# Kernel tuning notes

Hardware: AMD Instinct MI355X
Metric: run time of the kernel (lower is better)

Reference implementation:

```python
import jax, jax.numpy as jnp
import numpy as np

DIM = 768
NUM_HEADS = 12
HEAD_DIM = DIM // NUM_HEADS
SCALE = HEAD_DIM ** -0.5
B, N = 4, 2048


def setup_inputs() -> dict:
    key = jax.random.key(0)
    k1, k2, k3 = jax.random.split(key, 3)
    x = jax.random.normal(k1, (B, N, DIM), dtype=jnp.float32)
    W_qk = jax.random.normal(k2, (2 * DIM, DIM), dtype=jnp.float32) * (DIM ** -0.5)
    b_qk = jax.random.normal(k3, (2 * DIM,), dtype=jnp.float32) * 0.02
    return {"x": x, "W_qk": W_qk, "b_qk": b_qk}


def reference(x, W_qk, b_qk):
    Bb, Nn, C = x.shape
    # qk projection: [B,N,2C] -> [B,N,2,H,D] -> q,k each [B,H,N,D]
    qk = x @ W_qk.T + b_qk
    qk = qk.reshape(Bb, Nn, 2, NUM_HEADS, HEAD_DIM).transpose(2, 0, 3, 1, 4)
    q, k = qk[0], qk[1]
    # attention scores [B,H,N,N]
    attn = jnp.einsum("bhnd,bhmd->bhnm", q, k) * SCALE
    attn = jax.nn.softmax(attn, axis=-1)
    # mean over heads, then per-query diagonal -> [B,N]
    attn_weights = jnp.diagonal(attn.mean(axis=1), axis1=-2, axis2=-1)
    return attn_weights
```

## Files before the change

kernel.cpp:

```cpp
#include <hip/hip_runtime.h>
#include <math.h>


#define B_ 4
#define N_ 2048
#define H_ 12
#define D_ 64
#define C_ 768
#define TWO_C 1536
#define QSCALE 0.18033688011112043f

typedef _Float16 half8 __attribute__((ext_vector_type(8)));
typedef _Float16 half4 __attribute__((ext_vector_type(4)));
typedef float floatx4 __attribute__((ext_vector_type(4)));

#if __has_builtin(__builtin_amdgcn_exp2f)
#define EXP2(x) __builtin_amdgcn_exp2f(x)
#else
#define EXP2(x) exp2f(x)
#endif

__device__ __forceinline__ void gload_lds16(const _Float16* g, _Float16* l) {
  __builtin_amdgcn_global_load_lds(
      (const __attribute__((address_space(1))) void*)g,
      (__attribute__((address_space(3))) void*)l, 16, 0, 0);
}

#define NX4 1572864
#define NW4 294912
__global__ __launch_bounds__(256) void conv_kernel(const float* __restrict__ x,
                                                   const float* __restrict__ W,
                                                   _Float16* __restrict__ xh,
                                                   _Float16* __restrict__ wh) {
  int i = blockIdx.x * 256 + threadIdx.x;
  const float* in;
  _Float16* out;
  int idx;
  if (i < NX4) {
    in = x; out = xh; idx = i;
  } else if (i < NX4 + NW4) {
    in = W; out = wh; idx = i - NX4;
  } else {
    return;
  }
  float4 v = ((const float4*)in)[idx];
  half4 o;
  o[0] = (_Float16)v.x; o[1] = (_Float16)v.y;
  o[2] = (_Float16)v.z; o[3] = (_Float16)v.w;
  ((half4*)out)[idx] = o;
}

__global__ __launch_bounds__(256) void proj_kernel(
    const _Float16* __restrict__ xh, const _Float16* __restrict__ wh,
    const float* __restrict__ bias, _Float16* __restrict__ qh,
    _Float16* __restrict__ kh) {
  __shared__ _Float16 As[128 * 32];
  __shared__ _Float16 Bs[128 * 32];
  const int t = threadIdx.x;
  const int l = t & 63;
  const int w = t >> 6;
  const int wr = w >> 1, wc = w & 1;

  int lin = blockIdx.y * 12 + blockIdx.x;
  int swz = (lin & 7) * 96 + (lin >> 3);
  const int bm = (swz / 12) * 128;
  const int bc = (swz % 12) * 128;

  const int srow = l >> 2;
  const int schunk = (l & 3) ^ ((l >> 3) & 3);

  floatx4 acc[4][4] = {};

  for (int k0 = 0; k0 < C_; k0 += 32) {
    __syncthreads();
#pragma unroll
    for (int i = 0; i < 2; ++i) {
      int rbase = w * 32 + i * 16;
      const _Float16* ga =
          xh + (size_t)(bm + rbase + srow) * C_ + k0 + schunk * 8;
      gload_lds16(ga, As + rbase * 32);
      const _Float16* gb =
          wh + (size_t)(bc + rbase + srow) * C_ + k0 + schunk * 8;
      gload_lds16(gb, Bs + rbase * 32);
    }
    __syncthreads();

    half8 af[4], bf[4];
#pragma unroll
    for (int fr = 0; fr < 4; ++fr) {
      int row = wr * 64 + fr * 16 + (l & 15);
      int ch = (l >> 4) ^ ((row >> 1) & 3);
      af[fr] = *(const half8*)(As + row * 32 + ch * 8);
    }
#pragma unroll
    for (int fc = 0; fc < 4; ++fc) {
      int row = wc * 64 + fc * 16 + (l & 15);
      int ch = (l >> 4) ^ ((row >> 1) & 3);
      bf[fc] = *(const half8*)(Bs + row * 32 + ch * 8);
    }
#pragma unroll
    for (int fr = 0; fr < 4; ++fr)
#pragma unroll
      for (int fc = 0; fc < 4; ++fc)
        acc[fr][fc] = __builtin_amdgcn_mfma_f32_16x16x32_f16(
            af[fr], bf[fc], acc[fr][fc], 0, 0, 0);
  }

#pragma unroll
  for (int fr = 0; fr < 4; ++fr) {
#pragma unroll
    for (int fc = 0; fc < 4; ++fc) {
#pragma unroll
      for (int j = 0; j < 4; ++j) {
        int m = bm + wr * 64 + fr * 16 + ((l >> 4) << 2) + j;
        int c = bc + wc * 64 + fc * 16 + (l & 15);
        float v = acc[fr][fc][j] + bias[c];
        int b = m >> 11, n = m & (N_ - 1);
        int cc = (c < C_) ? c : c - C_;
        if (c < C_) v *= QSCALE;
        int hh = cc >> 6, d = cc & 63;
        _Float16* dst = (c < C_) ? qh : kh;
        dst[((((size_t)b * H_ + hh) * N_ + n) << 6) + d] = (_Float16)v;
      }
    }
  }
}

__global__ __launch_bounds__(256) void attn_kernel(
    const _Float16* __restrict__ qh, const _Float16* __restrict__ kh,
    float* __restrict__ part) {
  __shared__ _Float16 ks[4][64 * 64];
  const int t = threadIdx.x;
  const int l = t & 63;
  const int w = t >> 6;

  int lin = blockIdx.x;
  int swz = (lin & 7) * 192 + (lin >> 3);
  const int qt = swz & 31;
  const int h = (swz >> 5) % 12;
  const int b = swz / 384;

  const _Float16* qb = qh + (((size_t)(b * H_ + h) * N_ + qt * 64) << 6);
  const _Float16* kb = kh + (((size_t)(b * H_ + h) * N_) << 6);

  half8 qf[4][2];
#pragma unroll
  for (int fr = 0; fr < 4; ++fr)
#pragma unroll
    for (int kd = 0; kd < 2; ++kd)
      qf[fr][kd] = *(const half8*)(qb + (size_t)(fr * 16 + (l & 15)) * 64 +
                                   kd * 32 + (l >> 4) * 8);

  const int lin0 = w * 64 + l;
  const int row0 = lin0 >> 3, slot0 = lin0 & 7;
  const int soff0 = row0 * 64 + (slot0 ^ (row0 & 7)) * 8;
  const int lin1 = lin0 + 256;
  const int row1 = lin1 >> 3, slot1 = lin1 & 7;
  const int soff1 = row1 * 64 + (slot1 ^ (row1 & 7)) * 8;

#define STAGE(KT)                                                   \
  {                                                                 \
    const _Float16* kp_ = kb + (size_t)(KT) * 4096;                 \
    _Float16* ld_ = ks[(KT) & 3];                                   \
    gload_lds16(kp_ + soff0, ld_ + w * 512);                        \
    gload_lds16(kp_ + soff1, ld_ + w * 512 + 2048);                 \
  }

  const int frow = w * 16 + (l & 15);
  const int koff0 = frow * 64 + (((l >> 4) + 0) ^ (l & 7)) * 8;
  const int koff1 = frow * 64 + (((l >> 4) + 4) ^ (l & 7)) * 8;

  float lsum[4][4] = {};
  float ed[4] = {0.f, 0.f, 0.f, 0.f};

  STAGE(0);
  STAGE(1);
  STAGE(2);

#define ITER(KT, VMASM, DO_STAGE)                                             \
  {                                                                           \
    asm volatile(VMASM ::: "memory");                                         \
    __builtin_amdgcn_s_barrier();                                             \
    asm volatile("" ::: "memory");                                            \
    const _Float16* bufp = ks[(KT) & 3];                                      \
    half8 kf0 = *(const half8*)(bufp + koff0);                                \
    half8 kf1 = *(const half8*)(bufp + koff1);                                \
    if (DO_STAGE) STAGE((KT) + 3);                                            \
    floatx4 acc[4] = {};                                                      \
    _Pragma("unroll") for (int fr = 0; fr < 4; ++fr) {                        \
      acc[fr] = __builtin_amdgcn_mfma_f32_16x16x32_f16(qf[fr][0], kf0,        \
                                                       acc[fr], 0, 0, 0);     \
      acc[fr] = __builtin_amdgcn_mfma_f32_16x16x32_f16(qf[fr][1], kf1,        \
                                                       acc[fr], 0, 0, 0);     \
    }                                                                         \
    _Pragma("unroll") for (int fr = 0; fr < 4; ++fr)                          \
        _Pragma("unroll") for (int j = 0; j < 4; ++j) {                       \
      float e = EXP2(acc[fr][j]);                                             \
      lsum[fr][j] += e;                                                       \
    }                                                                         \
    if ((KT) == qt) {                                                         \
      _Pragma("unroll") for (int fr = 0; fr < 4; ++fr)                        \
          _Pragma("unroll") for (int j = 0; j < 4; ++j) {                     \
        if (fr == w && (l & 15) == (((l >> 4) << 2) + j))                     \
          ed[j] = EXP2(acc[fr][j]);                                           \
      }                                                                       \
    }                                                                         \
  }

  for (int kt = 0; kt < 29; ++kt) ITER(kt, "s_waitcnt vmcnt(4)", true);
  ITER(29, "s_waitcnt vmcnt(4)", false);
  ITER(30, "s_waitcnt vmcnt(2)", false);
  ITER(31, "s_waitcnt vmcnt(0)", false);
#undef ITER
#undef STAGE

#pragma unroll
  for (int fr = 0; fr < 4; ++fr)
#pragma unroll
    for (int j = 0; j < 4; ++j)
#pragma unroll
      for (int m = 1; m < 16; m <<= 1)
        lsum[fr][j] += __shfl_xor(lsum[fr][j], m, 16);
#pragma unroll
  for (int j = 0; j < 4; ++j)
#pragma unroll
    for (int m = 1; m < 16; m <<= 1) ed[j] += __shfl_xor(ed[j], m, 16);

  __builtin_amdgcn_s_barrier();
  float* red = (float*)ks[0];
  float* edl = red + 256;
  if ((l & 15) == 0) {
#pragma unroll
    for (int fr = 0; fr < 4; ++fr)
#pragma unroll
      for (int j = 0; j < 4; ++j)
        red[w * 64 + fr * 16 + ((l >> 4) << 2) + j] = lsum[fr][j];
#pragma unroll
    for (int j = 0; j < 4; ++j) edl[w * 16 + ((l >> 4) << 2) + j] = ed[j];
  }
  __syncthreads();

  if (t < 64) {
    float ls = red[t] + red[64 + t] + red[128 + t] + red[192 + t];
    part[(size_t)(b * H_ + h) * N_ + qt * 64 + t] = edl[t] / ls;
  }
}

__global__ __launch_bounds__(256) void reduce_kernel(
    const float* __restrict__ part, float* __restrict__ out) {
  int g = blockIdx.x * 256 + threadIdx.x;
  if (g >= B_ * N_) return;
  int b = g >> 11, n = g & (N_ - 1);
  float s = 0.0f;
#pragma unroll
  for (int hh = 0; hh < H_; ++hh) s += part[(size_t)(b * H_ + hh) * N_ + n];
  out[g] = s * (1.0f / (float)H_);
}

extern "C" void kernel_launch(void* const* d_in, const int* in_sizes, int n_in,
                              void* d_out, int out_size, void* d_ws,
                              size_t ws_size, hipStream_t stream) {
  const float* x = (const float*)d_in[0];
  const float* W = (const float*)d_in[1];
  const float* bias = (const float*)d_in[2];
  float* out = (float*)d_out;

  char* ws = (char*)d_ws;
  _Float16* xh = (_Float16*)ws;
  _Float16* wh = (_Float16*)(ws + 12582912);
  _Float16* qh = (_Float16*)(ws + 14942208);
  _Float16* kh = (_Float16*)(ws + 27525120);
  float* part = (float*)(ws + 40108032);

  conv_kernel<<<(NX4 + NW4 + 255) / 256, 256, 0, stream>>>(x, W, xh, wh);
  proj_kernel<<<dim3(TWO_C / 128, 8192 / 128), 256, 0, stream>>>(xh, wh, bias,
                                                                 qh, kh);
  attn_kernel<<<N_ / 64 * H_ * B_, 256, 0, stream>>>(qh, kh, part);
  reduce_kernel<<<(B_ * N_ + 255) / 256, 256, 0, stream>>>(part, out);
}
```

Before: 83.17 us.

## Triple-buffer projection GEMM loads and give each attention wave private K buffers

The projection GEMM moves from a single shared-memory buffer with two barriers per k-step to a 3-slot ring filled two stages ahead by async global-to-LDS loads. A vmcnt wait plus one barrier guards each stage, so load latency overlaps MFMA work. In the attention kernel each wave now stages its own 16-row K slice into a private LDS region laid out in fragment order. This removes the per-iteration block barrier and the XOR swizzle, leaving only per-wave vmcnt waits. The cost is more LDS in the projection kernel, which may lower occupancy, plus a plain linear LDS layout that could bring bank conflicts.

```diff
diff --git a/kernel.cpp b/kernel.cpp
--- a/kernel.cpp
+++ b/kernel.cpp
@@ -54,8 +54,8 @@
     const _Float16* __restrict__ xh, const _Float16* __restrict__ wh,
     const float* __restrict__ bias, _Float16* __restrict__ qh,
     _Float16* __restrict__ kh) {
-  __shared__ _Float16 As[128 * 32];
-  __shared__ _Float16 Bs[128 * 32];
+  __shared__ _Float16 As[3][128 * 32];
+  __shared__ _Float16 Bs[3][128 * 32];
   const int t = threadIdx.x;
   const int l = t & 63;
   const int w = t >> 6;
@@ -71,40 +71,52 @@
 
   floatx4 acc[4][4] = {};
 
-  for (int k0 = 0; k0 < C_; k0 += 32) {
-    __syncthreads();
-#pragma unroll
-    for (int i = 0; i < 2; ++i) {
-      int rbase = w * 32 + i * 16;
-      const _Float16* ga =
-          xh + (size_t)(bm + rbase + srow) * C_ + k0 + schunk * 8;
-      gload_lds16(ga, As + rbase * 32);
-      const _Float16* gb =
-          wh + (size_t)(bc + rbase + srow) * C_ + k0 + schunk * 8;
-      gload_lds16(gb, Bs + rbase * 32);
-    }
-    __syncthreads();
-
-    half8 af[4], bf[4];
-#pragma unroll
-    for (int fr = 0; fr < 4; ++fr) {
-      int row = wr * 64 + fr * 16 + (l & 15);
-      int ch = (l >> 4) ^ ((row >> 1) & 3);
-      af[fr] = *(const half8*)(As + row * 32 + ch * 8);
-    }
-#pragma unroll
-    for (int fc = 0; fc < 4; ++fc) {
-      int row = wc * 64 + fc * 16 + (l & 15);
-      int ch = (l >> 4) ^ ((row >> 1) & 3);
-      bf[fc] = *(const half8*)(Bs + row * 32 + ch * 8);
-    }
-#pragma unroll
-    for (int fr = 0; fr < 4; ++fr)
-#pragma unroll
-      for (int fc = 0; fc < 4; ++fc)
-        acc[fr][fc] = __builtin_amdgcn_mfma_f32_16x16x32_f16(
-            af[fr], bf[fc], acc[fr][fc], 0, 0, 0);
-  }
+#define PSTAGE(KT)                                                          \
+  {                                                                         \
+    const int sl_ = (KT) % 3;                                               \
+    const int k0_ = (KT) * 32;                                              \
+    _Pragma("unroll") for (int i_ = 0; i_ < 2; ++i_) {                      \
+      int rb_ = w * 32 + i_ * 16;                                           \
+      gload_lds16(xh + (size_t)(bm + rb_ + srow) * C_ + k0_ + schunk * 8,   \
+                  As[sl_] + rb_ * 32);                                      \
+      gload_lds16(wh + (size_t)(bc + rb_ + srow) * C_ + k0_ + schunk * 8,   \
+                  Bs[sl_] + rb_ * 32);                                      \
+    }                                                                       \
+  }
+
+#define PITER(KT, VMASM, DO_STAGE)                                          \
+  {                                                                         \
+    asm volatile(VMASM ::: "memory");                                       \
+    __builtin_amdgcn_s_barrier();                                           \
+    asm volatile("" ::: "memory");                                          \
+    const int sl_ = (KT) % 3;                                               \
+    const _Float16* Ap_ = As[sl_];                                          \
+    const _Float16* Bp_ = Bs[sl_];                                          \
+    half8 af[4], bf[4];                                                     \
+    _Pragma("unroll") for (int fr = 0; fr < 4; ++fr) {                      \
+      int row = wr * 64 + fr * 16 + (l & 15);                               \
+      int ch = (l >> 4) ^ ((row >> 1) & 3);                                 \
+      af[fr] = *(const half8*)(Ap_ + row * 32 + ch * 8);                    \
+    }                                                                       \
+    _Pragma("unroll") for (int fc = 0; fc < 4; ++fc) {                      \
+      int row = wc * 64 + fc * 16 + (l & 15);                               \
+      int ch = (l >> 4) ^ ((row >> 1) & 3);                                 \
+      bf[fc] = *(const half8*)(Bp_ + row * 32 + ch * 8);                    \
+    }                                                                       \
+    if (DO_STAGE) PSTAGE((KT) + 2);                                         \
+    _Pragma("unroll") for (int fr = 0; fr < 4; ++fr)                        \
+        _Pragma("unroll") for (int fc = 0; fc < 4; ++fc) acc[fr][fc] =      \
+        __builtin_amdgcn_mfma_f32_16x16x32_f16(af[fr], bf[fc],              \
+                                               acc[fr][fc], 0, 0, 0);       \
+  }
+
+  PSTAGE(0);
+  PSTAGE(1);
+  for (int kt = 0; kt < 22; ++kt) PITER(kt, "s_waitcnt vmcnt(4)", true);
+  PITER(22, "s_waitcnt vmcnt(4)", false);
+  PITER(23, "s_waitcnt vmcnt(0)", false);
+#undef PITER
+#undef PSTAGE
 
 #pragma unroll
   for (int fr = 0; fr < 4; ++fr) {
@@ -129,7 +141,7 @@
 __global__ __launch_bounds__(256) void attn_kernel(
     const _Float16* __restrict__ qh, const _Float16* __restrict__ kh,
     float* __restrict__ part) {
-  __shared__ _Float16 ks[4][64 * 64];
+  __shared__ _Float16 ks[4][4][1024];
   const int t = threadIdx.x;
   const int l = t & 63;
   const int w = t >> 6;
@@ -151,24 +163,15 @@
       qf[fr][kd] = *(const half8*)(qb + (size_t)(fr * 16 + (l & 15)) * 64 +
                                    kd * 32 + (l >> 4) * 8);
 
-  const int lin0 = w * 64 + l;
-  const int row0 = lin0 >> 3, slot0 = lin0 & 7;
-  const int soff0 = row0 * 64 + (slot0 ^ (row0 & 7)) * 8;
-  const int lin1 = lin0 + 256;
-  const int row1 = lin1 >> 3, slot1 = lin1 & 7;
-  const int soff1 = row1 * 64 + (slot1 ^ (row1 & 7)) * 8;
+  const _Float16* ksrc = kb + (w * 16 + (l & 15)) * 64 + (l >> 4) * 8;
 
 #define STAGE(KT)                                                   \
   {                                                                 \
-    const _Float16* kp_ = kb + (size_t)(KT) * 4096;                 \
-    _Float16* ld_ = ks[(KT) & 3];                                   \
-    gload_lds16(kp_ + soff0, ld_ + w * 512);                        \
-    gload_lds16(kp_ + soff1, ld_ + w * 512 + 2048);                 \
-  }
-
-  const int frow = w * 16 + (l & 15);
-  const int koff0 = frow * 64 + (((l >> 4) + 0) ^ (l & 7)) * 8;
-  const int koff1 = frow * 64 + (((l >> 4) + 4) ^ (l & 7)) * 8;
+    const _Float16* kp_ = ksrc + (size_t)(KT) * 4096;               \
+    _Float16* ld_ = &ks[w][(KT) & 3][0];                            \
+    gload_lds16(kp_, ld_);                                          \
+    gload_lds16(kp_ + 32, ld_ + 512);                               \
+  }
 
   float lsum[4][4] = {};
   float ed[4] = {0.f, 0.f, 0.f, 0.f};
@@ -180,11 +183,9 @@
 #define ITER(KT, VMASM, DO_STAGE)                                             \
   {                                                                           \
     asm volatile(VMASM ::: "memory");                                         \
-    __builtin_amdgcn_s_barrier();                                             \
-    asm volatile("" ::: "memory");                                            \
-    const _Float16* bufp = ks[(KT) & 3];                                      \
-    half8 kf0 = *(const half8*)(bufp + koff0);                                \
-    half8 kf1 = *(const half8*)(bufp + koff1);                                \
+    const _Float16* bufp = &ks[w][(KT) & 3][0];                               \
+    half8 kf0 = *(const half8*)(bufp + l * 8);                                \
+    half8 kf1 = *(const half8*)(bufp + 512 + l * 8);                          \
     if (DO_STAGE) STAGE((KT) + 3);                                            \
     floatx4 acc[4] = {};                                                      \
     _Pragma("unroll") for (int fr = 0; fr < 4; ++fr) {                        \
@@ -226,8 +227,8 @@
 #pragma unroll
     for (int m = 1; m < 16; m <<= 1) ed[j] += __shfl_xor(ed[j], m, 16);
 
-  __builtin_amdgcn_s_barrier();
-  float* red = (float*)ks[0];
+  __syncthreads();
+  float* red = (float*)&ks[0][0][0];
   float* edl = red + 256;
   if ((l & 15) == 0) {
 #pragma unroll
```

New measurement: 93.43 us. 1.12x slower.
